# Optimization experiments

Measured on AMD Instinct MI355X. Metric: run time of the kernel, lower is better.

## Reference

```python
import jax, jax.numpy as jnp
import numpy as np

B, NQ, NK = 4, 1024, 1024
DQ, DK, DO = 1024, 1024, 1024
H = 16
HIDDEN = 2048  # mlp_ratio=2.0


def dyt(x, alpha, gamma):
    # DyT: gamma * tanh(alpha * x), gamma broadcast over last (channel) dim for 3D input
    return gamma[None, None, :] * jnp.tanh(alpha * x)


def setup_inputs() -> dict:
    key = jax.random.key(0)
    ks = jax.random.split(key, 12)
    s = lambda d: 1.0 / np.sqrt(d)
    return {
        "xk": jax.random.normal(ks[0], (B, NK, DK), jnp.float32),
        "xq": jax.random.normal(ks[1], (B, NQ, DQ), jnp.float32),
        "alpha_q": jnp.float32(0.5), "gamma_q": jnp.ones((DQ,), jnp.float32),
        "alpha_k": jnp.float32(0.5), "gamma_k": jnp.ones((DK,), jnp.float32),
        "Wq": jax.random.normal(ks[2], (DQ, DO), jnp.float32) * s(DQ),
        "Wkv": jax.random.normal(ks[3], (DK, 2 * DO), jnp.float32) * s(DK),
        "Wproj": jax.random.normal(ks[4], (DO, DO), jnp.float32) * s(DO),
        "bproj": jnp.zeros((DO,), jnp.float32),
        "alpha2": jnp.float32(0.5), "gamma2": jnp.ones((DO,), jnp.float32),
        "W1": jax.random.normal(ks[5], (DO, HIDDEN), jnp.float32) * s(DO),
        "b1": jnp.zeros((HIDDEN,), jnp.float32),
        "W2": jax.random.normal(ks[6], (HIDDEN, DO), jnp.float32) * s(HIDDEN),
        "b2": jnp.zeros((DO,), jnp.float32),
    }


def reference(xk, xq, alpha_q, gamma_q, alpha_k, gamma_k, Wq, Wkv, Wproj, bproj,
              alpha2, gamma2, W1, b1, W2, b2):
    head_dim = DO // H
    scale = head_dim ** -0.5
    # DyT pre-norms
    xk_n = dyt(xk, alpha_k, gamma_k)
    xq_n = dyt(xq, alpha_q, gamma_q)
    # projections (qkv_bias=False)
    q = (xq_n @ Wq).reshape(B, NQ, H, head_dim)          # bqhd
    kv = (xk_n @ Wkv).reshape(B, NK, 2, H, head_dim)
    k, v = kv[:, :, 0], kv[:, :, 1]                       # bkhd
    attn = jax.nn.softmax(jnp.einsum('bqhd,bkhd->bhqk', q, k) * scale, axis=-1)
    o = jnp.einsum('bhqk,bkhd->bqhd', attn, v).reshape(B, NQ, DO)
    x = o @ Wproj + bproj
    # MLP with residual (drop_path/dropout are identity in eval)
    h = dyt(x, alpha2, gamma2)
    h = jax.nn.gelu(h @ W1 + b1, approximate=False)
    h = h @ W2 + b2
    return x + h
```

## Files before the change

kernel.cpp:

```cpp
#include <hip/hip_runtime.h>
#include <hip/hip_fp16.h>
#include <cstdint>

typedef _Float16 f16x8 __attribute__((ext_vector_type(8)));
typedef _Float16 f16x4 __attribute__((ext_vector_type(4)));
typedef float    f32x4 __attribute__((ext_vector_type(4)));
typedef float    f32x16 __attribute__((ext_vector_type(16)));

__device__ __forceinline__ f32x4 mfma16(f16x8 a, f16x8 b, f32x4 c) {
  return __builtin_amdgcn_mfma_f32_16x16x32_f16(a, b, c, 0, 0, 0);
}
__device__ __forceinline__ f32x16 mfma32(f16x8 a, f16x8 b, f32x16 c) {
  return __builtin_amdgcn_mfma_f32_32x32x16_f16(a, b, c, 0, 0, 0);
}
__device__ __forceinline__ void gload_lds16(const void* g, void* l) {
  __builtin_amdgcn_global_load_lds(
      (const __attribute__((address_space(1))) void*)g,
      (__attribute__((address_space(3))) void*)l, 16, 0, 0);
}
__device__ __forceinline__ unsigned pkrtz(float a, float b) {
  auto h2 = __builtin_amdgcn_cvt_pkrtz(a, b);
  return __builtin_bit_cast(unsigned, h2);
}

__device__ __forceinline__ void wtrans_tile256(
    const float* __restrict__ S, _Float16* __restrict__ D,
    int R, int C, int bx, int by, float sc, float* tle )
{
  int tx = threadIdx.x & 31, ty = threadIdx.x >> 5;
  int x = bx * 32 + tx;
#pragma unroll
  for (int j = 0; j < 4; ++j) {
    int y = by * 32 + ty + j * 8;
    tle[(ty + j * 8) * 33 + tx] = S[(size_t)y * C + x];
  }
  __syncthreads();
  int xo = by * 32 + tx;
#pragma unroll
  for (int j = 0; j < 4; ++j) {
    int yo = bx * 32 + ty + j * 8;
    D[(size_t)yo * R + xo] = (_Float16)(tle[tx * 33 + ty + j * 8] * sc);
  }
}

__global__ __launch_bounds__(256) void prep_kernel(
    const float* __restrict__ Xq, const float* __restrict__ Xk,
    const float* __restrict__ aq, const float* __restrict__ gq,
    const float* __restrict__ ak, const float* __restrict__ gk,
    _Float16* __restrict__ Yq, _Float16* __restrict__ Yk,
    const float* __restrict__ Wq, const float* __restrict__ Wkv,
    _Float16* __restrict__ WqT, _Float16* __restrict__ WkvT,
    const float* __restrict__ Wproj, const float* __restrict__ W1,
    const float* __restrict__ W2,
    _Float16* __restrict__ WprojT, _Float16* __restrict__ W1T,
    _Float16* __restrict__ W2T)
{
  if (blockIdx.x < 8192) {
    int i = blockIdx.x * 256 + threadIdx.x;
    const float* X; const float* gamma; float a; _Float16* Y;
    if (i < 1048576) { X = Xq; gamma = gq; a = aq[0]; Y = Yq; }
    else { i -= 1048576; X = Xk; gamma = gk; a = ak[0]; Y = Yk; }
    float4 v = ((const float4*)X)[i];
    int c = (i * 4) & 1023;
    f16x4 o;
    o[0] = (_Float16)(gamma[c + 0] * tanhf(a * v.x));
    o[1] = (_Float16)(gamma[c + 1] * tanhf(a * v.y));
    o[2] = (_Float16)(gamma[c + 2] * tanhf(a * v.z));
    o[3] = (_Float16)(gamma[c + 3] * tanhf(a * v.w));
    *(f16x4*)(Y + (size_t)i * 4) = o;
  } else {
    __shared__ float tle[32 * 33];
    int t = blockIdx.x - 8192;
    const float* S; _Float16* D; int R, C; float sc = 1.0f;
    if (t < 1024)      { S = Wq;    D = WqT;    R = 1024; C = 1024; sc = 0.18033688011112042f; }
    else if (t < 3072) { S = Wkv;   D = WkvT;   R = 1024; C = 2048; t -= 1024; }
    else if (t < 4096) { S = Wproj; D = WprojT; R = 1024; C = 1024; t -= 3072; }
    else if (t < 6144) { S = W1;    D = W1T;    R = 1024; C = 2048; t -= 4096; }
    else               { S = W2;    D = W2T;    R = 2048; C = 1024; t -= 6144; }
    const int tilesX = C >> 5;
    wtrans_tile256(S, D, R, C, t % tilesX, t / tilesX, sc, tle);
  }
}

template <int EPI>
__device__ __forceinline__ void gemm_body(
    _Float16* smem,
    const _Float16* __restrict__ A, const _Float16* __restrict__ BT,
    int N, int K, int bm, int bn,
    _Float16* __restrict__ C16, _Float16* __restrict__ X16,
    const float* __restrict__ bias, const float* __restrict__ alpha_p,
    const float* __restrict__ gamma, const _Float16* __restrict__ resid16,
    float* __restrict__ outf)
{
  const int tid = threadIdx.x;
  const int w = tid >> 6, l = tid & 63;
  const int g = l >> 4, r = l & 15;
  const int wm = w >> 1, wn = w & 1;
  const int srow = tid >> 2;
  const int skey = (tid >> 3) & 3;
  const int scol = ((tid & 3) ^ skey) << 3;

  const _Float16* gA = A + (size_t)(bm + srow) * K + scol;
  const _Float16* gB = BT + (size_t)(bn + srow) * K + scol;
  char* dA = (char*)smem + tid * 16;
  char* dB = (char*)smem + 8192 + tid * 16;

  const int rk = (r >> 1) & 3;
  const int gsw = (g ^ rk) << 3;

  f32x4 acc[2][4] = {};
  const int KT = K >> 5;

  auto stage = [&](int buf) {
    gload_lds16(gA, dA + buf * 16384);
    gload_lds16(gB, dB + buf * 16384);
    gA += 32; gB += 32;
  };

  stage(0);
  stage(1);

  int cur = 0;
  for (int kt = 0; kt < KT; ++kt) {
    if (kt < KT - 1) asm volatile("s_waitcnt vmcnt(2) lgkmcnt(0)" ::: "memory");
    else             asm volatile("s_waitcnt vmcnt(0) lgkmcnt(0)" ::: "memory");
    __builtin_amdgcn_s_barrier();
    asm volatile("" ::: "memory");
    if (kt + 2 < KT) { int b2 = cur + 2; if (b2 >= 3) b2 -= 3; stage(b2); }
    const _Float16* Asc = smem + cur * 8192;
    const _Float16* Bsc = Asc + 4096;
    f16x8 af[2], bf[4];
#pragma unroll
    for (int m = 0; m < 2; ++m)
      af[m] = *(const f16x8*)(Asc + (wm * 32 + m * 16 + r) * 32 + gsw);
#pragma unroll
    for (int n = 0; n < 4; ++n)
      bf[n] = *(const f16x8*)(Bsc + (wn * 64 + n * 16 + r) * 32 + gsw);
    __builtin_amdgcn_s_setprio(1);
#pragma unroll
    for (int m = 0; m < 2; ++m)
#pragma unroll
      for (int n = 0; n < 4; ++n)
        acc[m][n] = mfma16(af[m], bf[n], acc[m][n]);
    __builtin_amdgcn_s_setprio(0);
    ++cur; if (cur == 3) cur = 0;
  }

  const int row0 = bm + wm * 32 + 4 * g;
  const int col0 = bn + wn * 64 + r;

  if constexpr (EPI == 5) {
    if (bn < 1024) {
#pragma unroll
      for (int m = 0; m < 2; ++m)
#pragma unroll
        for (int n = 0; n < 4; ++n)
#pragma unroll
          for (int rr = 0; rr < 4; ++rr)
            C16[(size_t)(row0 + m * 16 + rr) * 1024 + col0 + n * 16] =
                (_Float16)acc[m][n][rr];
    } else {
#pragma unroll
      for (int m = 0; m < 2; ++m) {
        const int row = row0 + m * 16;
        const int bq = row >> 10, nk = row & 1023;
#pragma unroll
        for (int n = 0; n < 4; ++n) {
          const int vcol = col0 + n * 16 - 1024;
          f16x4 t;
#pragma unroll
          for (int rr = 0; rr < 4; ++rr) t[rr] = (_Float16)acc[m][n][rr];
          *(f16x4*)(X16 + ((size_t)((bq << 4) + (vcol >> 6)) * 64 + (vcol & 63)) * 1024 + nk) = t;
        }
      }
    }
    return;
  }

#pragma unroll
  for (int m = 0; m < 2; ++m) {
#pragma unroll
    for (int n = 0; n < 4; ++n) {
#pragma unroll
      for (int rr = 0; rr < 4; ++rr) {
        const int row = row0 + m * 16 + rr;
        const int col = col0 + n * 16;
        const size_t idx = (size_t)row * N + col;
        float v = acc[m][n][rr];
        if constexpr (EPI == 0) {
          C16[idx] = (_Float16)v;
        } else if constexpr (EPI == 2) {
          float x = v + bias[col];
          X16[idx] = (_Float16)x;
          C16[idx] = (_Float16)(gamma[col] * tanhf(alpha_p[0] * x));
        } else if constexpr (EPI == 3) {
          float tt = v + bias[col];
          C16[idx] = (_Float16)(0.5f * tt * (1.0f + erff(tt * 0.7071067811865475f)));
        } else {
          outf[idx] = (float)resid16[idx] + v + bias[col];
        }
      }
    }
  }
}

template <int EPI>
__global__ __launch_bounds__(512, 6) void gemm_f16(
    const _Float16* __restrict__ A, const _Float16* __restrict__ BT,
    int N, int K, int nTnShift,
    _Float16* __restrict__ C16, _Float16* __restrict__ X16,
    const float* __restrict__ bias, const float* __restrict__ alpha_p,
    const float* __restrict__ gamma, const _Float16* __restrict__ resid16,
    float* __restrict__ outf)
{
  __shared__ __align__(16) _Float16 smem[24576];
  const int chunk = gridDim.x >> 3;
  const int bid = ((int)blockIdx.x & 7) * chunk + ((int)blockIdx.x >> 3);
  const int bm = (bid >> nTnShift) << 7;
  const int bn = (bid & ((1 << nTnShift) - 1)) << 7;
  gemm_body<EPI>(smem, A, BT, N, K, bm, bn,
                 C16, X16, bias, alpha_p, gamma, resid16, outf);
}

__global__ __launch_bounds__(512, 6) void gemm_qkv(
    const _Float16* __restrict__ Aq, const _Float16* __restrict__ Bq,
    _Float16* __restrict__ Cq,
    const _Float16* __restrict__ Ak, const _Float16* __restrict__ Bk,
    _Float16* __restrict__ K16, _Float16* __restrict__ VT)
{
  __shared__ __align__(16) _Float16 smem[24576];
  int bid = ((int)blockIdx.x & 7) * 96 + ((int)blockIdx.x >> 3);
  if (bid < 256) {
    gemm_body<0>(smem, Aq, Bq, 1024, 1024, (bid >> 3) << 7, (bid & 7) << 7,
                 Cq, nullptr, nullptr, nullptr, nullptr, nullptr, nullptr);
  } else {
    bid -= 256;
    gemm_body<5>(smem, Ak, Bk, 2048, 1024, (bid >> 4) << 7, (bid & 15) << 7,
                 K16, VT, nullptr, nullptr, nullptr, nullptr, nullptr);
  }
}

__global__ __launch_bounds__(256) void attn_kernel(
    const _Float16* __restrict__ Q, const _Float16* __restrict__ K16,
    const _Float16* __restrict__ VT, _Float16* __restrict__ O)
{
  __shared__ __align__(16) char smemc[65536];

  const int tid = threadIdx.x;

  const int bid = ((int)blockIdx.x & 7) * 64 + ((int)blockIdx.x >> 3);
  const int qb = bid & 7, hh = (bid >> 3) & 15, b = bid >> 7;
  const int w = tid >> 6, l = tid & 63;
  const int r = l & 31, h2 = l >> 5;
  const int q0 = qb * 128 + w * 32;

  f16x8 qf[4];
  {
    const _Float16* qp = Q + (size_t)(b * 1024 + q0 + r) * 1024 + hh * 64 + 8 * h2;
#pragma unroll
    for (int s = 0; s < 4; ++s) qf[s] = *(const f16x8*)(qp + s * 16);
  }

  f16x8 onef;
#pragma unroll
  for (int i = 0; i < 8; ++i) onef[i] = (_Float16)1.0f;

  f32x16 oacc0 = {}, oacc1 = {}, lacc = {};

  const int srow = tid >> 3, sslot = tid & 7;
  const int swz = (sslot ^ (srow & 7)) << 3;
  const _Float16* kbase = K16 + (size_t)(b * 1024 + srow) * 1024 + hh * 64 + swz;
  const _Float16* vbase = VT + ((size_t)((b * 16 + hh) * 64) + srow) * 1024 + swz;
  char* kd0 = (char*)smemc + tid * 16;
  char* vd0 = (char*)smemc + 8192 + tid * 16;

  auto stage = [&](int t) {
    const size_t kb = (size_t)(t << 6);
    const int buf = t & 3;
    char* kd = kd0 + buf * 16384;
    char* vd = vd0 + buf * 16384;
#pragma unroll
    for (int j = 0; j < 2; ++j)
      gload_lds16(kbase + (kb + 32 * j) * 1024, kd + j * 4096);
#pragma unroll
    for (int j = 0; j < 2; ++j)
      gload_lds16(vbase + (size_t)(32 * j) * 1024 + kb, vd + j * 4096);
  };

  stage(0);
  stage(1);

  const int rsw0 = r & 7;

  for (int kt = 0; kt < 16; ++kt) {
    if (kt + 2 < 16) stage(kt + 2);
    if (kt < 14)       asm volatile("s_waitcnt vmcnt(8)" ::: "memory");
    else if (kt == 14) asm volatile("s_waitcnt vmcnt(4)" ::: "memory");
    else               asm volatile("s_waitcnt vmcnt(0)" ::: "memory");
    __builtin_amdgcn_s_barrier();
    asm volatile("" ::: "memory");

    const _Float16* Kc = (const _Float16*)(smemc + (kt & 3) * 16384);
    const _Float16* Vc = Kc + 4096;

    f32x16 s0 = {}, s1 = {};
    __builtin_amdgcn_s_setprio(1);
#pragma unroll
    for (int s = 0; s < 4; ++s) {
      const int cch = 2 * s + h2;
      f16x8 a0 = *(const f16x8*)(Kc + r * 64 + ((cch ^ rsw0) << 3));
      f16x8 a1 = *(const f16x8*)(Kc + (32 + r) * 64 + ((cch ^ rsw0) << 3));
      s0 = mfma32(a0, qf[s], s0);
      s1 = mfma32(a1, qf[s], s1);
    }
    __builtin_amdgcn_s_setprio(0);

#pragma unroll
    for (int i = 0; i < 16; ++i) s0[i] = __builtin_amdgcn_exp2f(s0[i]);
#pragma unroll
    for (int i = 0; i < 16; ++i) s1[i] = __builtin_amdgcn_exp2f(s1[i]);

    unsigned own[16];
#pragma unroll
    for (int u = 0; u < 8; ++u) {
      const int tb = (u & 3) * 4;
      if (u < 4) {
        own[2 * u]     = pkrtz(s0[tb], s0[tb + 1]);
        own[2 * u + 1] = pkrtz(s0[tb + 2], s0[tb + 3]);
      } else {
        own[2 * u]     = pkrtz(s1[tb], s1[tb + 1]);
        own[2 * u + 1] = pkrtz(s1[tb + 2], s1[tb + 3]);
      }
    }
    f16x8 pf[4];
#pragma unroll
    for (int s = 0; s < 4; ++s) {
      auto r0 = __builtin_amdgcn_permlane32_swap(own[4 * s], own[4 * s + 2], false, false);
      auto r1 = __builtin_amdgcn_permlane32_swap(own[4 * s + 1], own[4 * s + 3], false, false);
      union { unsigned u[4]; f16x8 v; } fu;
      fu.u[0] = r0[0]; fu.u[1] = r1[0]; fu.u[2] = r0[1]; fu.u[3] = r1[1];
      pf[s] = fu.v;
    }

    __builtin_amdgcn_s_setprio(1);
#pragma unroll
    for (int s = 0; s < 4; ++s) {
      const int cch = 2 * s + h2;
      f16x8 va = *(const f16x8*)(Vc + r * 64 + ((cch ^ rsw0) << 3));
      f16x8 vb = *(const f16x8*)(Vc + (32 + r) * 64 + ((cch ^ rsw0) << 3));
      oacc0 = mfma32(va, pf[s], oacc0);
      oacc1 = mfma32(vb, pf[s], oacc1);
      lacc  = mfma32(onef, pf[s], lacc);
    }
    __builtin_amdgcn_s_setprio(0);
    asm volatile("" ::: "memory");
  }

  const float inv = 1.0f / lacc[0];
  _Float16* op = O + (size_t)(b * 1024 + q0 + r) * 1024 + hh * 64 + 4 * h2;
#pragma unroll
  for (int u = 0; u < 4; ++u) {
    f16x4 t0, t1;
#pragma unroll
    for (int v = 0; v < 4; ++v) {
      t0[v] = (_Float16)(oacc0[4 * u + v] * inv);
      t1[v] = (_Float16)(oacc1[4 * u + v] * inv);
    }
    *(f16x4*)(op + 8 * u) = t0;
    *(f16x4*)(op + 32 + 8 * u) = t1;
  }
}

extern "C" void kernel_launch(void* const* d_in, const int* in_sizes, int n_in,
                              void* d_out, int out_size, void* d_ws, size_t ws_size,
                              hipStream_t stream)
{
  const float* xk      = (const float*)d_in[0];
  const float* xq      = (const float*)d_in[1];
  const float* alpha_q = (const float*)d_in[2];
  const float* gamma_q = (const float*)d_in[3];
  const float* alpha_k = (const float*)d_in[4];
  const float* gamma_k = (const float*)d_in[5];
  const float* Wq      = (const float*)d_in[6];
  const float* Wkv     = (const float*)d_in[7];
  const float* Wproj   = (const float*)d_in[8];
  const float* bproj   = (const float*)d_in[9];
  const float* alpha2  = (const float*)d_in[10];
  const float* gamma2  = (const float*)d_in[11];
  const float* W1      = (const float*)d_in[12];
  const float* b1      = (const float*)d_in[13];
  const float* W2      = (const float*)d_in[14];
  const float* b2      = (const float*)d_in[15];

  char* p = (char*)d_ws;
  _Float16* xqn    = (_Float16*)p; p += 8388608;
  _Float16* xkn    = (_Float16*)p; p += 8388608;
  _Float16* WqT    = (_Float16*)p; p += 2097152;
  _Float16* WkvT   = (_Float16*)p; p += 4194304;
  _Float16* WprojT = (_Float16*)p; p += 2097152;
  _Float16* W1T    = (_Float16*)p; p += 4194304;
  _Float16* W2T    = (_Float16*)p; p += 4194304;
  _Float16* q16    = (_Float16*)p; p += 8388608;
  _Float16* vt16   = (_Float16*)p; p += 8388608;
  _Float16* k16    = (_Float16*)p; p += 8388608;
  _Float16* h16    = (_Float16*)p; p += 16777216;
  _Float16* o16    = (_Float16*)p; p += 8388608;
  _Float16* x16  = q16;
  _Float16* g16  = xqn;
  float*    outf = (float*)d_out;

  prep_kernel<<<16384, 256, 0, stream>>>(xq, xk, alpha_q, gamma_q, alpha_k, gamma_k,
      xqn, xkn, Wq, Wkv, WqT, WkvT, Wproj, W1, W2, WprojT, W1T, W2T);
  gemm_qkv<<<768, 512, 0, stream>>>(xqn, WqT, q16, xkn, WkvT, k16, vt16);
  attn_kernel<<<512, 256, 0, stream>>>(q16, k16, vt16, o16);
  gemm_f16<2><<<256, 512, 0, stream>>>(o16, WprojT, 1024, 1024, 3,
      g16, x16, bproj, alpha2, gamma2, nullptr, nullptr);
  gemm_f16<3><<<512, 512, 0, stream>>>(g16, W1T, 2048, 1024, 4,
      h16, nullptr, b1, nullptr, nullptr, nullptr, nullptr);
  gemm_f16<4><<<256, 512, 0, stream>>>(h16, W2T, 1024, 2048, 3,
      nullptr, nullptr, b2, nullptr, nullptr, x16, outf);
}
```

Before: 160.0 us.

## Split attention KV range in two with a separate combine kernel

Splits each attention block's 1024 keys into two halves handled by separate blocks, doubling the grid to 1024 blocks. Each writes unnormalized fp32 partial outputs and row sums into reused workspace, and a new combine kernel adds them and normalizes to fp16. The pipeline also drops from 4-stage to 2-stage double buffering with full waits, halving LDS to raise occupancy. The cost is an extra launch and extra fp32 traffic for the partials, plus a shallower prefetch depth.

```diff
diff --git a/kernel.cpp b/kernel.cpp
--- a/kernel.cpp
+++ b/kernel.cpp
@@ -242,17 +242,21 @@
 
 __global__ __launch_bounds__(256) void attn_kernel(
     const _Float16* __restrict__ Q, const _Float16* __restrict__ K16,
-    const _Float16* __restrict__ VT, _Float16* __restrict__ O)
-{
-  __shared__ __align__(16) char smemc[65536];
+    const _Float16* __restrict__ VT,
+    float* __restrict__ PO0, float* __restrict__ PO1,
+    float* __restrict__ Lbuf )
+{
+  __shared__ __align__(16) char smemc[32768];
 
   const int tid = threadIdx.x;
 
-  const int bid = ((int)blockIdx.x & 7) * 64 + ((int)blockIdx.x >> 3);
-  const int qb = bid & 7, hh = (bid >> 3) & 15, b = bid >> 7;
+  const int bid = ((int)blockIdx.x & 7) * 128 + ((int)blockIdx.x >> 3);
+  const int h = bid & 1, qb = (bid >> 1) & 7, hh = (bid >> 4) & 15, b = bid >> 8;
   const int w = tid >> 6, l = tid & 63;
   const int r = l & 31, h2 = l >> 5;
   const int q0 = qb * 128 + w * 32;
+
+  float* PO = h ? PO1 : PO0;
 
   f16x8 qf[4];
   {
@@ -274,9 +278,8 @@
   char* kd0 = (char*)smemc + tid * 16;
   char* vd0 = (char*)smemc + 8192 + tid * 16;
 
-  auto stage = [&](int t) {
-    const size_t kb = (size_t)(t << 6);
-    const int buf = t & 3;
+  auto stage = [&](int t, int buf) {
+    const size_t kb = (size_t)((h * 8 + t) << 6);
     char* kd = kd0 + buf * 16384;
     char* vd = vd0 + buf * 16384;
 #pragma unroll
@@ -287,20 +290,18 @@
       gload_lds16(vbase + (size_t)(32 * j) * 1024 + kb, vd + j * 4096);
   };
 
-  stage(0);
-  stage(1);
+  stage(0, 0);
 
   const int rsw0 = r & 7;
-
-  for (int kt = 0; kt < 16; ++kt) {
-    if (kt + 2 < 16) stage(kt + 2);
-    if (kt < 14)       asm volatile("s_waitcnt vmcnt(8)" ::: "memory");
-    else if (kt == 14) asm volatile("s_waitcnt vmcnt(4)" ::: "memory");
-    else               asm volatile("s_waitcnt vmcnt(0)" ::: "memory");
+  int cur = 0;
+
+  for (int kt = 0; kt < 8; ++kt) {
+    asm volatile("s_waitcnt vmcnt(0) lgkmcnt(0)" ::: "memory");
     __builtin_amdgcn_s_barrier();
     asm volatile("" ::: "memory");
-
-    const _Float16* Kc = (const _Float16*)(smemc + (kt & 3) * 16384);
+    if (kt + 1 < 8) stage(kt + 1, cur ^ 1);
+
+    const _Float16* Kc = (const _Float16*)(smemc + cur * 16384);
     const _Float16* Vc = Kc + 4096;
 
     f32x16 s0 = {}, s1 = {};
@@ -353,22 +354,47 @@
       lacc  = mfma32(onef, pf[s], lacc);
     }
     __builtin_amdgcn_s_setprio(0);
-    asm volatile("" ::: "memory");
-  }
-
-  const float inv = 1.0f / lacc[0];
-  _Float16* op = O + (size_t)(b * 1024 + q0 + r) * 1024 + hh * 64 + 4 * h2;
+
+    __builtin_amdgcn_s_barrier();
+    cur ^= 1;
+  }
+
+  float* op = PO + (size_t)(b * 1024 + q0 + r) * 1024 + hh * 64 + 4 * h2;
 #pragma unroll
   for (int u = 0; u < 4; ++u) {
-    f16x4 t0, t1;
-#pragma unroll
-    for (int v = 0; v < 4; ++v) {
-      t0[v] = (_Float16)(oacc0[4 * u + v] * inv);
-      t1[v] = (_Float16)(oacc1[4 * u + v] * inv);
-    }
-    *(f16x4*)(op + 8 * u) = t0;
-    *(f16x4*)(op + 32 + 8 * u) = t1;
-  }
+    f32x4 t0, t1;
+#pragma unroll
+    for (int v = 0; v < 4; ++v) { t0[v] = oacc0[4 * u + v]; t1[v] = oacc1[4 * u + v]; }
+    *(f32x4*)(op + 8 * u) = t0;
+    *(f32x4*)(op + 32 + 8 * u) = t1;
+  }
+  if (h2 == 0)
+    Lbuf[h * 65536 + (b * 16 + hh) * 1024 + q0 + r] = lacc[0];
+}
+
+__global__ __launch_bounds__(256) void combine_kernel(
+    const float* __restrict__ PO0, const float* __restrict__ PO1,
+    const float* __restrict__ Lbuf, _Float16* __restrict__ O)
+{
+  const int i = (int)blockIdx.x * 256 + threadIdx.x;
+  const size_t base = (size_t)i * 8;
+  const int c = (int)(base & 1023);
+  const int q = (int)((base >> 10) & 1023);
+  const int b = (int)(base >> 20);
+  const int hh = c >> 6;
+  const int li = (b * 16 + hh) * 1024 + q;
+  const float inv = 1.0f / (Lbuf[li] + Lbuf[65536 + li]);
+  f32x4 a0 = *(const f32x4*)(PO0 + base);
+  f32x4 a1 = *(const f32x4*)(PO0 + base + 4);
+  f32x4 b0 = *(const f32x4*)(PO1 + base);
+  f32x4 b1 = *(const f32x4*)(PO1 + base + 4);
+  f16x8 o;
+#pragma unroll
+  for (int j = 0; j < 4; ++j) {
+    o[j]     = (_Float16)((a0[j] + b0[j]) * inv);
+    o[4 + j] = (_Float16)((a1[j] + b1[j]) * inv);
+  }
+  *(f16x8*)(O + base) = o;
 }
 
 extern "C" void kernel_launch(void* const* d_in, const int* in_sizes, int n_in,
@@ -405,6 +431,9 @@
   _Float16* k16    = (_Float16*)p; p += 8388608;
   _Float16* h16    = (_Float16*)p; p += 16777216;
   _Float16* o16    = (_Float16*)p; p += 8388608;
+  float*    po0  = (float*)h16;
+  float*    po1  = (float*)d_ws;
+  float*    lbuf = (float*)WqT;
   _Float16* x16  = q16;
   _Float16* g16  = xqn;
   float*    outf = (float*)d_out;
@@ -412,7 +441,8 @@
   prep_kernel<<<16384, 256, 0, stream>>>(xq, xk, alpha_q, gamma_q, alpha_k, gamma_k,
       xqn, xkn, Wq, Wkv, WqT, WkvT, Wproj, W1, W2, WprojT, W1T, W2T);
   gemm_qkv<<<768, 512, 0, stream>>>(xqn, WqT, q16, xkn, WkvT, k16, vt16);
-  attn_kernel<<<512, 256, 0, stream>>>(q16, k16, vt16, o16);
+  attn_kernel<<<1024, 256, 0, stream>>>(q16, k16, vt16, po0, po1, lbuf);
+  combine_kernel<<<2048, 256, 0, stream>>>(po0, po1, lbuf, o16);
   gemm_f16<2><<<256, 512, 0, stream>>>(o16, WprojT, 1024, 1024, 3,
       g16, x16, bproj, alpha2, gamma2, nullptr, nullptr);
   gemm_f16<3><<<512, 512, 0, stream>>>(g16, W1T, 2048, 1024, 4,
```

Result: slower. 169.3 us (+5.8%).
